# Performance work log

Hardware: AMD Instinct MI355X
Metric: run time of the kernel (lower is better)

The kernel has to match this reference:

```python
import jax, jax.numpy as jnp
import numpy as np

N = 50000          # num nodes
E = 800000         # num edges
IN_C, HID_C, OUT_C = 128, 256, 256
LN_EPS = 1e-5


def gcn_conv(x, W, b, row, col):
    """PyG GCNConv: h = D^{-1/2}(A+I)D^{-1/2} (x W) + b, self-loops added."""
    h = x @ W                                             # [N, C_out]
    deg = jax.ops.segment_sum(jnp.ones((row.shape[0],), h.dtype), col,
                              num_segments=N) + 1.0        # +1 for self-loop
    dinv = jax.lax.rsqrt(deg)                              # [N]
    msg = h[row] * (dinv[row] * dinv[col])[:, None]        # [E, C_out] gathered msgs
    agg = jax.ops.segment_sum(msg, col, num_segments=N)
    agg = agg + h * (dinv * dinv)[:, None]                 # self-loop contribution
    return agg + b


def layer_norm(x, gamma, beta):
    mu = jnp.mean(x, axis=-1, keepdims=True)
    var = jnp.mean(jnp.square(x - mu), axis=-1, keepdims=True)
    return (x - mu) * jax.lax.rsqrt(var + LN_EPS) * gamma + beta


def setup_inputs() -> dict:
    key = jax.random.key(0)
    ks = jax.random.split(key, 8)
    x = jax.random.normal(ks[0], (N, IN_C), jnp.float32)
    edge_index = jax.random.randint(ks[1], (2, E), 0, N, dtype=jnp.int64)
    W1 = jax.random.normal(ks[2], (IN_C, HID_C), jnp.float32) * (1.0 / np.sqrt(IN_C))
    b1 = jnp.zeros((HID_C,), jnp.float32)
    W2 = jax.random.normal(ks[3], (HID_C, OUT_C), jnp.float32) * (1.0 / np.sqrt(HID_C))
    b2 = jnp.zeros((OUT_C,), jnp.float32)
    ln1_g = jnp.ones((HID_C,), jnp.float32); ln1_b = jnp.zeros((HID_C,), jnp.float32)
    ln2_g = jnp.ones((OUT_C,), jnp.float32); ln2_b = jnp.zeros((OUT_C,), jnp.float32)
    proj_W = jax.random.normal(ks[4], (IN_C, OUT_C), jnp.float32) * (1.0 / np.sqrt(IN_C))
    proj_b = jnp.zeros((OUT_C,), jnp.float32)
    return {"x": x, "edge_index": edge_index, "W1": W1, "b1": b1, "W2": W2,
            "b2": b2, "ln1_g": ln1_g, "ln1_b": ln1_b, "ln2_g": ln2_g,
            "ln2_b": ln2_b, "proj_W": proj_W, "proj_b": proj_b}


def reference(x, edge_index, W1, b1, W2, b2, ln1_g, ln1_b, ln2_g, ln2_b,
              proj_W, proj_b):
    row, col = edge_index[0], edge_index[1]   # messages flow row -> col
    identity = x @ proj_W + proj_b            # self.proj (Linear, in != out)
    h = gcn_conv(x, W1, b1, row, col)
    h = jax.nn.relu(layer_norm(h, ln1_g, ln1_b))   # dropout = identity (eval)
    g = gcn_conv(h, W2, b2, row, col)
    g = layer_norm(g, ln2_g, ln2_b)
    return jax.nn.relu(g + identity)
```

## Files before the change

### kernel.cpp

```cpp
#include <hip/hip_runtime.h>

#define NN 50000
#define NE 800000
#define LN_EPS 1e-5f

using bf16x8 = __attribute__((ext_vector_type(8))) short;
using f32x4  = __attribute__((ext_vector_type(4))) float;

__device__ __forceinline__ float b2f(unsigned short u) {
    union { unsigned int i; float f; } c;
    c.i = ((unsigned int)u) << 16;
    return c.f;
}
__device__ __forceinline__ unsigned short f2b(float f) {
    union { float f; unsigned int i; } c;
    c.f = f;
    const unsigned int i = c.i;
    return (unsigned short)((i + 0x7FFFu + ((i >> 16) & 1u)) >> 16);
}

template <int ITERS>
__device__ __forceinline__ void stage_async(const short* __restrict__ g,
                                            short* __restrict__ l) {
    const int lane = threadIdx.x & 63;
    const int wv = threadIdx.x >> 6;
#pragma unroll
    for (int i = 0; i < ITERS; ++i) {
        const int u = i * 256 + wv * 64;
        __builtin_amdgcn_global_load_lds(
            (const __attribute__((address_space(1))) void*)(g + (size_t)(u + lane) * 8),
            (__attribute__((address_space(3))) void*)(l + (size_t)u * 8),
            16, 0, 0);
    }
}

template <int K>
__device__ __forceinline__ void pack_body(const float* __restrict__ W,
                                          short* __restrict__ Wp, int i) {
    constexpr int KB = K / 32;
    const int j = i & 7;
    const int l = (i >> 3) & 63;
    const int t = i >> 9;
    const int kb = t % KB;
    const int nt = t / KB;
    const int k = 32 * kb + 8 * (l >> 4) + j;
    const int n = 16 * nt + (l & 15);
    Wp[i] = (short)f2b(W[(size_t)k * 256 + n]);
}

__global__ __launch_bounds__(256) void prep_k(
    const float* __restrict__ x, const float* __restrict__ W1,
    const float* __restrict__ W2, const float* __restrict__ pW,
    short* __restrict__ xb, short* __restrict__ Wp1,
    short* __restrict__ Wp2, short* __restrict__ Wpp) {
    const int b = blockIdx.x;
    if (b < 6250) {
        const int i = b * 256 + threadIdx.x;
        const float4 v = ((const float4*)x)[i];
        ushort4 o;
        o.x = f2b(v.x); o.y = f2b(v.y); o.z = f2b(v.z); o.w = f2b(v.w);
        ((ushort4*)xb)[i] = o;
    } else if (b < 6250 + 128) {
        pack_body<128>(W1, Wp1, (b - 6250) * 256 + threadIdx.x);
    } else if (b < 6250 + 384) {
        pack_body<256>(W2, Wp2, (b - 6378) * 256 + threadIdx.x);
    } else {
        pack_body<128>(pW, Wpp, (b - 6634) * 256 + threadIdx.x);
    }
}

__global__ __launch_bounds__(256) void count_k(const int* __restrict__ col,
                                               int* __restrict__ rowptr) {
    const int e = blockIdx.x * 256 + threadIdx.x;
    if (e < NE) atomicAdd(&rowptr[col[e] + 1], 1);
}

__global__ __launch_bounds__(256) void block_sum_k(const int* __restrict__ p,
                                                   int* __restrict__ psum, int n) {
    __shared__ int sh[256];
    const int t = threadIdx.x;
    const int i = blockIdx.x * 256 + t;
    sh[t] = (i < n) ? p[i] : 0;
    __syncthreads();
#pragma unroll
    for (int off = 128; off > 0; off >>= 1) {
        if (t < off) sh[t] += sh[t + off];
        __syncthreads();
    }
    if (t == 0) psum[blockIdx.x] = sh[0];
}

__global__ __launch_bounds__(256) void scan_apply_k(int* __restrict__ p,
                                                    const int* __restrict__ psum,
                                                    float* __restrict__ dinv,
                                                    int n, int nblk) {
    __shared__ int sh[256];
    const int t = threadIdx.x;
    const int b = blockIdx.x;
    const int i = b * 256 + t;
    sh[t] = (t < b && t < nblk) ? psum[t] : 0;
    __syncthreads();
#pragma unroll
    for (int off = 128; off > 0; off >>= 1) {
        if (t < off) sh[t] += sh[t + off];
        __syncthreads();
    }
    const int carry = sh[0];
    __syncthreads();
    const int raw = (i < n) ? p[i] : 0;
    if (i >= 1 && i < n) dinv[i - 1] = rsqrtf((float)raw + 1.0f);
    sh[t] = raw;
    __syncthreads();
#pragma unroll
    for (int off = 1; off < 256; off <<= 1) {
        const int u = (t >= off) ? sh[t - off] : 0;
        __syncthreads();
        sh[t] += u;
        __syncthreads();
    }
    if (i < n) p[i] = sh[t] + carry;
}

__global__ __launch_bounds__(256) void fill_k(const int* __restrict__ row,
                                              const int* __restrict__ col,
                                              const float* __restrict__ dinv,
                                              int* __restrict__ rowptr,
                                              int2* __restrict__ pairs) {
    const int e = blockIdx.x * 256 + threadIdx.x;
    if (e >= NE) return;
    const int rr = row[e];
    const int pos = atomicAdd(&rowptr[col[e]], 1);
    int2 pr;
    pr.x = rr;
    pr.y = __float_as_int(dinv[rr]);
    pairs[pos] = pr;
}

__global__ __launch_bounds__(256) void gather1_k(const short* __restrict__ X,
                                                 const int* __restrict__ endptr,
                                                 const int2* __restrict__ pairs,
                                                 const float* __restrict__ dinv,
                                                 short* __restrict__ A1) {
    const int node = blockIdx.x * 4 + (threadIdx.x >> 6);
    const int lane = threadIdx.x & 63;
    if (node >= NN) return;
    const int start = node ? endptr[node - 1] : 0;
    const int end = endptr[node];

    float a0 = 0.f, a1 = 0.f;
    int j = start;
    for (; j + 7 < end; j += 8) {
        int2 p[8];
        ushort2 v[8];
#pragma unroll
        for (int u = 0; u < 8; ++u) p[u] = pairs[j + u];
#pragma unroll
        for (int u = 0; u < 8; ++u)
            v[u] = ((const ushort2*)(X + (size_t)p[u].x * 128))[lane];
#pragma unroll
        for (int u = 0; u < 8; ++u) {
            const float w = __int_as_float(p[u].y);
            a0 += b2f(v[u].x) * w;
            a1 += b2f(v[u].y) * w;
        }
    }
    for (; j < end; ++j) {
        const int2 p0 = pairs[j];
        const float w0 = __int_as_float(p0.y);
        const ushort2 v0 = ((const ushort2*)(X + (size_t)p0.x * 128))[lane];
        a0 += b2f(v0.x) * w0;
        a1 += b2f(v0.y) * w0;
    }
    const float dc = dinv[node];
    const ushort2 h = ((const ushort2*)(X + (size_t)node * 128))[lane];
    a0 = (a0 + b2f(h.x) * dc) * dc;
    a1 = (a1 + b2f(h.y) * dc) * dc;
    ushort2 o;
    o.x = f2b(a0); o.y = f2b(a1);
    ((ushort2*)A1)[(size_t)node * 64 + lane] = o;
}

__global__ __launch_bounds__(256) void gather2_k(const short* __restrict__ H,
                                                 const int* __restrict__ endptr,
                                                 const int2* __restrict__ pairs,
                                                 const float* __restrict__ dinv,
                                                 short* __restrict__ agg) {
    const int node = blockIdx.x * 4 + (threadIdx.x >> 6);
    const int lane = threadIdx.x & 63;
    if (node >= NN) return;
    const int start = node ? endptr[node - 1] : 0;
    const int end = endptr[node];

    float a0 = 0.f, a1 = 0.f, a2 = 0.f, a3 = 0.f;
    int j = start;
    for (; j + 7 < end; j += 8) {
        int2 p[8];
        ushort4 v[8];
#pragma unroll
        for (int u = 0; u < 8; ++u) p[u] = pairs[j + u];
#pragma unroll
        for (int u = 0; u < 8; ++u)
            v[u] = ((const ushort4*)(H + (size_t)p[u].x * 256))[lane];
#pragma unroll
        for (int u = 0; u < 8; ++u) {
            const float w = __int_as_float(p[u].y);
            a0 += b2f(v[u].x) * w;
            a1 += b2f(v[u].y) * w;
            a2 += b2f(v[u].z) * w;
            a3 += b2f(v[u].w) * w;
        }
    }
    for (; j < end; ++j) {
        const int2 p0 = pairs[j];
        const float w0 = __int_as_float(p0.y);
        const ushort4 v0 = ((const ushort4*)(H + (size_t)p0.x * 256))[lane];
        a0 += b2f(v0.x) * w0;
        a1 += b2f(v0.y) * w0;
        a2 += b2f(v0.z) * w0;
        a3 += b2f(v0.w) * w0;
    }
    const float dc = dinv[node];
    const ushort4 h = ((const ushort4*)(H + (size_t)node * 256))[lane];
    ushort4 o;
    o.x = f2b((a0 + b2f(h.x) * dc) * dc);
    o.y = f2b((a1 + b2f(h.y) * dc) * dc);
    o.z = f2b((a2 + b2f(h.z) * dc) * dc);
    o.w = f2b((a3 + b2f(h.w) * dc) * dc);
    ((ushort4*)agg)[(size_t)node * 64 + lane] = o;
}

template <int K, bool PROJ, bool OUT_BF16>
__global__ __launch_bounds__(256) void gemm_ln_k(
    const short* __restrict__ X, const short* __restrict__ Wp,
    const float* __restrict__ bias, const float* __restrict__ gamma,
    const float* __restrict__ beta, const short* __restrict__ Xp,
    const short* __restrict__ Wpp, const float* __restrict__ pbias,
    void* __restrict__ Yv) {
    constexpr int KB = K / 32;
    constexpr int NTC = 16 / KB;
    constexpr int NPH = 16 / NTC;
    constexpr int CHUNK = 8192;
    __shared__ short lds[2][CHUNK];
    const int lane = threadIdx.x & 63;
    const int wv = threadIdx.x >> 6;
    const int row0 = blockIdx.x * 64 + wv * 16;
    const int r = row0 + (lane & 15);
    const int rc = (r < NN) ? r : (NN - 1);
    const int kof = 8 * (lane >> 4);
    const int colbase = lane & 15;

    bf16x8 a[KB];
#pragma unroll
    for (int kb = 0; kb < KB; ++kb)
        a[kb] = *(const bf16x8*)(X + (size_t)rc * K + 32 * kb + kof);
    bf16x8 ap[4];
    if (PROJ) {
#pragma unroll
        for (int kb = 0; kb < 4; ++kb)
            ap[kb] = *(const bf16x8*)(Xp + (size_t)rc * 128 + 32 * kb + kof);
    }

    stage_async<4>(Wp, lds[0]);

    f32x4 acc[16];
#pragma unroll
    for (int c = 0; c < NPH; ++c) {
        __syncthreads();
        if (c < NPH - 1)
            stage_async<4>(Wp + (size_t)(c + 1) * CHUNK, lds[(c + 1) & 1]);
        else if (PROJ)
            stage_async<4>(Wpp, lds[(c + 1) & 1]);
        const short* buf = lds[c & 1];
#pragma unroll
        for (int ntl = 0; ntl < NTC; ++ntl) {
            f32x4 cacc = {0.f, 0.f, 0.f, 0.f};
#pragma unroll
            for (int kb = 0; kb < KB; ++kb) {
                const bf16x8 b = ((const bf16x8*)buf)[(ntl * KB + kb) * 64 + lane];
                cacc = __builtin_amdgcn_mfma_f32_16x16x32_bf16(a[kb], b, cacc, 0, 0, 0);
            }
            acc[c * NTC + ntl] = cacc;
        }
    }

    float s[4] = {0.f, 0.f, 0.f, 0.f};
    float q[4] = {0.f, 0.f, 0.f, 0.f};
#pragma unroll
    for (int nt = 0; nt < 16; ++nt) {
        const float bv = bias[nt * 16 + colbase];
#pragma unroll
        for (int rg = 0; rg < 4; ++rg) {
            const float v = acc[nt][rg] + bv;
            acc[nt][rg] = v;
            s[rg] += v;
            q[rg] += v * v;
        }
    }
#pragma unroll
    for (int off = 1; off < 16; off <<= 1) {
#pragma unroll
        for (int rg = 0; rg < 4; ++rg) {
            s[rg] += __shfl_xor(s[rg], off, 64);
            q[rg] += __shfl_xor(q[rg], off, 64);
        }
    }
    float mu[4], rsd[4];
#pragma unroll
    for (int rg = 0; rg < 4; ++rg) {
        mu[rg] = s[rg] * (1.f / 256.f);
        const float var = q[rg] * (1.f / 256.f) - mu[rg] * mu[rg];
        rsd[rg] = rsqrtf(var + LN_EPS);
    }

    const int orow0 = row0 + (lane >> 4) * 4;
    if (PROJ) {
#pragma unroll
        for (int pc = 0; pc < 4; ++pc) {
            __syncthreads();
            if (pc < 3)
                stage_async<4>(Wpp + (size_t)(pc + 1) * 8192, lds[(pc + 1) & 1]);
            const short* buf = lds[pc & 1];
#pragma unroll
            for (int ntl = 0; ntl < 4; ++ntl) {
                const int nt = pc * 4 + ntl;
                f32x4 pid = {0.f, 0.f, 0.f, 0.f};
#pragma unroll
                for (int kb = 0; kb < 4; ++kb) {
                    const bf16x8 b = ((const bf16x8*)buf)[(ntl * 4 + kb) * 64 + lane];
                    pid = __builtin_amdgcn_mfma_f32_16x16x32_bf16(ap[kb], b, pid, 0, 0, 0);
                }
                const int col = nt * 16 + colbase;
                const float g = gamma[col];
                const float be = beta[col];
                const float pbv = pbias[col];
#pragma unroll
                for (int rg = 0; rg < 4; ++rg) {
                    const int orow = orow0 + rg;
                    float v = (acc[nt][rg] - mu[rg]) * rsd[rg] * g + be;
                    v += pid[rg] + pbv;
                    v = fmaxf(v, 0.f);
                    if (orow < NN) {
                        if (OUT_BF16)
                            ((short*)Yv)[(size_t)orow * 256 + col] = (short)f2b(v);
                        else
                            ((float*)Yv)[(size_t)orow * 256 + col] = v;
                    }
                }
            }
        }
    } else {
#pragma unroll
        for (int nt = 0; nt < 16; ++nt) {
            const int col = nt * 16 + colbase;
            const float g = gamma[col];
            const float be = beta[col];
#pragma unroll
            for (int rg = 0; rg < 4; ++rg) {
                const int orow = orow0 + rg;
                float v = (acc[nt][rg] - mu[rg]) * rsd[rg] * g + be;
                v = fmaxf(v, 0.f);
                if (orow < NN) {
                    if (OUT_BF16)
                        ((short*)Yv)[(size_t)orow * 256 + col] = (short)f2b(v);
                    else
                        ((float*)Yv)[(size_t)orow * 256 + col] = v;
                }
            }
        }
    }
}

extern "C" void kernel_launch(void* const* d_in, const int* in_sizes, int n_in,
                              void* d_out, int out_size, void* d_ws, size_t ws_size,
                              hipStream_t stream) {
    const float* x    = (const float*)d_in[0];
    const int*   eidx = (const int*)d_in[1];
    const float* W1   = (const float*)d_in[2];
    const float* b1   = (const float*)d_in[3];
    const float* W2   = (const float*)d_in[4];
    const float* b2   = (const float*)d_in[5];
    const float* ln1g = (const float*)d_in[6];
    const float* ln1b = (const float*)d_in[7];
    const float* ln2g = (const float*)d_in[8];
    const float* ln2b = (const float*)d_in[9];
    const float* pW   = (const float*)d_in[10];
    const float* pb   = (const float*)d_in[11];

    const int* row = eidx;
    const int* col = eidx + NE;
    float* out = (float*)d_out;

    short* xb     = (short*)d_ws;
    short* A1     = xb + (size_t)NN * 128;
    short* Bb     = A1 + (size_t)NN * 128;
    short* Ag     = Bb + (size_t)NN * 256;
    float* dinv   = (float*)(Ag + (size_t)NN * 256);
    int*   rowptr = (int*)(dinv + NN);
    int*   psum   = rowptr + NN + 4;
    int2*  pairs  = (int2*)(psum + 256);
    short* Wp1    = (short*)(pairs + NE);
    short* Wp2    = Wp1 + 128 * 256;
    short* Wpp    = Wp2 + 256 * 256;

    const int nscan = NN + 1;
    const int nblk = (nscan + 255) / 256;

    hipMemsetAsync(rowptr, 0, (NN + 4) * sizeof(int), stream);
    prep_k<<<6762, 256, 0, stream>>>(x, W1, W2, pW, xb, Wp1, Wp2, Wpp);
    count_k<<<(NE + 255) / 256, 256, 0, stream>>>(col, rowptr);
    block_sum_k<<<nblk, 256, 0, stream>>>(rowptr, psum, nscan);
    scan_apply_k<<<nblk, 256, 0, stream>>>(rowptr, psum, dinv, nscan, nblk);
    fill_k<<<(NE + 255) / 256, 256, 0, stream>>>(row, col, dinv, rowptr, pairs);

    gather1_k<<<(NN + 3) / 4, 256, 0, stream>>>(xb, rowptr, pairs, dinv, A1);
    gemm_ln_k<128, false, true><<<(NN + 63) / 64, 256, 0, stream>>>(
        A1, Wp1, b1, ln1g, ln1b, nullptr, nullptr, nullptr, Bb);

    gather2_k<<<(NN + 3) / 4, 256, 0, stream>>>(Bb, rowptr, pairs, dinv, Ag);
    gemm_ln_k<256, true, false><<<(NN + 63) / 64, 256, 0, stream>>>(
        Ag, Wp2, b2, ln2g, ln2b, xb, Wpp, pb, out);
}
```

Measured before the change: 277.3 us.

## Replace atomic CSR fill with two-pass bucketed scatter by destination range

The single-pass CSR fill, which did scattered global atomics and writes for every edge, is replaced by two passes. The first pass bins edges into 98 coarse buckets by destination node (col>>9), using shared-memory counting and staging. The second pass processes one bucket per block, so the rowptr atomics and pair writes hit a localized address range with better cache locality. This adds an extra kernel launch and intermediate buffer traffic. It packs (col,row) into 16 bits each, which cannot hold node ids up to 50000 in col<<16 without overflow issues (col fits in 16 bits, but row up to 49999 also fits, so this is fine). Capping each bucket at 10240 entries risks silently dropping edges if a bucket overflows.

```diff
diff --git a/kernel.cpp b/kernel.cpp
--- a/kernel.cpp
+++ b/kernel.cpp
@@ -3,6 +3,12 @@
 #define NN 50000
 #define NE 800000
 #define LN_EPS 1e-5f
+
+#define BSHIFT 9
+#define NBUCK 98
+#define BCAP 10240
+#define CHUNK_E 8192
+#define NBLK_A ((NE + CHUNK_E - 1) / CHUNK_E)
 
 using bf16x8 = __attribute__((ext_vector_type(8))) short;
 using f32x4  = __attribute__((ext_vector_type(4))) float;
@@ -121,19 +127,89 @@
     if (i < n) p[i] = sh[t] + carry;
 }
 
-__global__ __launch_bounds__(256) void fill_k(const int* __restrict__ row,
-                                              const int* __restrict__ col,
-                                              const float* __restrict__ dinv,
-                                              int* __restrict__ rowptr,
-                                              int2* __restrict__ pairs) {
-    const int e = blockIdx.x * 256 + threadIdx.x;
-    if (e >= NE) return;
-    const int rr = row[e];
-    const int pos = atomicAdd(&rowptr[col[e]], 1);
-    int2 pr;
-    pr.x = rr;
-    pr.y = __float_as_int(dinv[rr]);
-    pairs[pos] = pr;
+__global__ __launch_bounds__(256) void bucketA_k(const int* __restrict__ row,
+                                                 const int* __restrict__ col,
+                                                 int* __restrict__ gcnt,
+                                                 unsigned int* __restrict__ gbuck) {
+    __shared__ unsigned int stage[CHUNK_E];
+    __shared__ int cnt[NBUCK];
+    __shared__ int bnd[NBUCK + 1];
+    __shared__ int boff[NBUCK];
+    __shared__ int gbase[NBUCK];
+    const int t = threadIdx.x;
+    const int e0 = blockIdx.x * CHUNK_E;
+    const int n = min(CHUNK_E, NE - e0);
+
+    for (int i = t; i < NBUCK; i += 256) cnt[i] = 0;
+    __syncthreads();
+    for (int i = t; i < n; i += 256)
+        atomicAdd(&cnt[col[e0 + i] >> BSHIFT], 1);
+    __syncthreads();
+    if (t == 0) {
+        int s = 0;
+        for (int b = 0; b < NBUCK; ++b) {
+            bnd[b] = s;
+            boff[b] = s;
+            s += cnt[b];
+        }
+        bnd[NBUCK] = s;
+    }
+    __syncthreads();
+    for (int b = t; b < NBUCK; b += 256)
+        gbase[b] = atomicAdd(&gcnt[b], cnt[b]);
+    for (int i = t; i < n; i += 256) {
+        const int c = col[e0 + i];
+        const int s = row[e0 + i];
+        const int p = atomicAdd(&boff[c >> BSHIFT], 1);
+        stage[p] = ((unsigned int)c << 16) | (unsigned int)s;
+    }
+    __syncthreads();
+    for (int i = t; i < n; i += 256) {
+        int lo = 0, hi = NBUCK;
+        while (hi - lo > 1) {
+            const int mid = (lo + hi) >> 1;
+            if (bnd[mid] <= i) lo = mid; else hi = mid;
+        }
+        const int off = gbase[lo] + (i - bnd[lo]);
+        gbuck[(size_t)lo * BCAP + min(off, BCAP - 1)] = stage[i];
+    }
+}
+
+__global__ __launch_bounds__(256) void bucketB_k(const unsigned int* __restrict__ gbuck,
+                                                 const int* __restrict__ gcnt,
+                                                 const float* __restrict__ dinv,
+                                                 int* __restrict__ rowptr,
+                                                 int2* __restrict__ pairs) {
+    const int b = blockIdx.x;
+    const int n = min(gcnt[b], BCAP);
+    const unsigned int* src = gbuck + (size_t)b * BCAP;
+    int i = threadIdx.x;
+    for (; i + 768 < n; i += 1024) {
+        const unsigned int u0 = src[i];
+        const unsigned int u1 = src[i + 256];
+        const unsigned int u2 = src[i + 512];
+        const unsigned int u3 = src[i + 768];
+        int2 a, bb, c, d;
+        a.x = (int)(u0 & 0xffffu);  a.y = __float_as_int(dinv[a.x]);
+        bb.x = (int)(u1 & 0xffffu); bb.y = __float_as_int(dinv[bb.x]);
+        c.x = (int)(u2 & 0xffffu);  c.y = __float_as_int(dinv[c.x]);
+        d.x = (int)(u3 & 0xffffu);  d.y = __float_as_int(dinv[d.x]);
+        const int p0 = atomicAdd(&rowptr[u0 >> 16], 1);
+        const int p1 = atomicAdd(&rowptr[u1 >> 16], 1);
+        const int p2 = atomicAdd(&rowptr[u2 >> 16], 1);
+        const int p3 = atomicAdd(&rowptr[u3 >> 16], 1);
+        pairs[p0] = a;
+        pairs[p1] = bb;
+        pairs[p2] = c;
+        pairs[p3] = d;
+    }
+    for (; i < n; i += 256) {
+        const unsigned int u = src[i];
+        int2 pr;
+        pr.x = (int)(u & 0xffffu);
+        pr.y = __float_as_int(dinv[pr.x]);
+        pairs[atomicAdd(&rowptr[u >> 16], 1)] = pr;
+    }
 }
 
 __global__ __launch_bounds__(256) void gather1_k(const short* __restrict__ X,
@@ -396,21 +472,24 @@
     short* Ag     = Bb + (size_t)NN * 256;
     float* dinv   = (float*)(Ag + (size_t)NN * 256);
     int*   rowptr = (int*)(dinv + NN);
-    int*   psum   = rowptr + NN + 4;
+    int*   gcnt   = rowptr + NN + 4;
+    int*   psum   = gcnt + 128;
     int2*  pairs  = (int2*)(psum + 256);
-    short* Wp1    = (short*)(pairs + NE);
+    unsigned int* gbuck = (unsigned int*)(pairs + NE);
+    short* Wp1    = (short*)(gbuck + (size_t)NBUCK * BCAP);
     short* Wp2    = Wp1 + 128 * 256;
     short* Wpp    = Wp2 + 256 * 256;
 
     const int nscan = NN + 1;
     const int nblk = (nscan + 255) / 256;
 
-    hipMemsetAsync(rowptr, 0, (NN + 4) * sizeof(int), stream);
+    hipMemsetAsync(rowptr, 0, (NN + 4 + 128) * sizeof(int), stream);
     prep_k<<<6762, 256, 0, stream>>>(x, W1, W2, pW, xb, Wp1, Wp2, Wpp);
     count_k<<<(NE + 255) / 256, 256, 0, stream>>>(col, rowptr);
     block_sum_k<<<nblk, 256, 0, stream>>>(rowptr, psum, nscan);
     scan_apply_k<<<nblk, 256, 0, stream>>>(rowptr, psum, dinv, nscan, nblk);
-    fill_k<<<(NE + 255) / 256, 256, 0, stream>>>(row, col, dinv, rowptr, pairs);
+    bucketA_k<<<NBLK_A, 256, 0, stream>>>(row, col, gcnt, gbuck);
+    bucketB_k<<<NBUCK, 256, 0, stream>>>(gbuck, gcnt, dinv, rowptr, pairs);
 
     gather1_k<<<(NN + 3) / 4, 256, 0, stream>>>(xb, rowptr, pairs, dinv, A1);
     gemm_ln_k<128, false, true><<<(NN + 63) / 64, 256, 0, stream>>>(
```

New measurement: 297.2 us. +7.2%, slower.
